# Kernel tuning notes

Hardware: AMD Instinct MI355X
Metric: run time of the kernel (lower is better)

## Reference

```python
import jax, jax.numpy as jnp
import numpy as np

N_BLADES = 8
GRADE = np.array([0, 1, 1, 1, 2, 2, 2, 3])
WEIGHT_EXPANSION = np.array([0, 1, 1, 1, 2, 2, 2, 3])
GRADE_BLADES = ([0], [1, 2, 3], [4, 5, 6], [7])
EPS = 1e-6


def _build_cayley():
    # Blades as bitmasks over generators e1,e2,e3; canonical order = sorted by (grade, mask)
    # -> [1, e1, e2, e3, e12, e13, e23, e123], matching weight_expansion [0,1,1,1,2,2,2,3].
    masks = sorted(range(8), key=lambda m: (bin(m).count('1'), m))
    m2i = {m: i for i, m in enumerate(masks)}
    ti, tj, tk, ts, triples = [], [], [], [], []
    for i, a in enumerate(masks):
        for j, b in enumerate(masks):
            # reorder sign for Euclidean Cl(3,0): count transpositions
            swaps = sum(bin(a >> (bit + 1)).count('1') for bit in range(3) if (b >> bit) & 1)
            k = m2i[a ^ b]
            ti.append(i); tj.append(j); tk.append(k)
            ts.append(-1.0 if swaps % 2 else 1.0)
            triples.append((int(GRADE[i]), int(GRADE[j]), int(GRADE[k])))
    uniq = sorted(set(triples))  # 20 directed grade-interaction paths for P3M0
    pidx = {t: p for p, t in enumerate(uniq)}
    tp = np.array([pidx[t] for t in triples])
    return (np.array(ti), np.array(tj), np.array(tk),
            np.array(ts, dtype=np.float32), tp, len(uniq))


TI, TJ, TK, TS, TP, NUM_PATHS = _build_cayley()  # NUM_PATHS == 20


def _forward(x, linear_weight, linear_bias, gp_weight, normalize=True):
    # grade-wise linear map via blade-expanded weights: y[k] = x[k] @ W[grade(k)] + b
    y = jnp.einsum('kbi,kio->kbo', x, linear_weight[WEIGHT_EXPANSION]) + linear_bias
    y = jax.nn.gelu(y, approximate=True)
    # steerable weighted geometric product: one learnable weight per feature per grade path
    wpath = gp_weight.T[TP]  # [64, F]: path weight for each blade-product term
    terms = (TS[:, None, None] * wpath[:, None, :]) * x[TI] * y[TJ]  # [64, B, F]
    out = jax.ops.segment_sum(terms, TK, num_segments=N_BLADES)  # [8, B, F]
    if normalize:
        # grade-wise RMS norm: per sample, normalize each grade subspace over its blades and features
        parts = []
        for blades in GRADE_BLADES:
            og = out[np.array(blades)]  # [n_blades_g, B, F]
            rms = jnp.sqrt(jnp.mean(og * og, axis=(0, 2), keepdims=True) + EPS)
            parts.append(og / rms)
        out = jnp.concatenate(parts, axis=0)
    return out


def setup_inputs() -> dict:
    key = jax.random.key(0)
    k1, k2, k3 = jax.random.split(key, 3)
    B, F = 4096, 512
    x = jax.random.normal(k1, (N_BLADES, B, F), dtype=jnp.float32)
    gp_weight = jax.random.normal(k2, (F, NUM_PATHS), dtype=jnp.float32) * np.float32(1.0 / np.sqrt(3 + 1))
    linear_weight = jax.random.normal(k3, (4, F, F), dtype=jnp.float32) * np.float32(1.0 / np.sqrt(F))
    linear_bias = jnp.zeros((1, 1, F), dtype=jnp.float32)
    return {"x": x, "linear_weight": linear_weight, "linear_bias": linear_bias, "gp_weight": gp_weight}


def reference(x, linear_weight, linear_bias, gp_weight):
    return _forward(x, linear_weight, linear_bias, gp_weight, normalize=True)
```

## Files before the change

### kernel.cpp

```cpp
#include <hip/hip_runtime.h>

typedef short short8v __attribute__((ext_vector_type(8)));
typedef float f32x4 __attribute__((ext_vector_type(4)));
typedef unsigned short u16;
typedef unsigned int u32;

__device__ __forceinline__ u16 f2bf(float f) {
    u32 u = __float_as_uint(f);
    u += 0x7FFFu + ((u >> 16) & 1u);
    return (u16)(u >> 16);
}
__device__ __forceinline__ float bf2f(u16 h) {
    return __uint_as_float(((u32)h) << 16);
}
__device__ __forceinline__ float gelu_f(float v) {
    float u = 0.7978845608028654f * fmaf(0.044715f * v, v * v, v);
    return 0.5f * v * (1.0f + tanhf(u));
}
__device__ __forceinline__ void gload16(const void* g, void* l) {
    __builtin_amdgcn_global_load_lds(
        (const __attribute__((address_space(1))) u32*)g,
        (__attribute__((address_space(3))) u32*)l, 16, 0, 0);
}

__global__ __launch_bounds__(256) void k_prep(const float* __restrict__ x, u16* __restrict__ xb,
                                              const float* __restrict__ w, u16* __restrict__ wt) {
    const int bid = blockIdx.x, tid = threadIdx.x;
    if (bid < 8192) {
        int idx = bid * 256 + tid;
        const float4* in = (const float4*)x;
        float4 a = in[idx * 2], c = in[idx * 2 + 1];
        short8v s;
        s[0] = (short)f2bf(a.x); s[1] = (short)f2bf(a.y); s[2] = (short)f2bf(a.z); s[3] = (short)f2bf(a.w);
        s[4] = (short)f2bf(c.x); s[5] = (short)f2bf(c.y); s[6] = (short)f2bf(c.z); s[7] = (short)f2bf(c.w);
        *(short8v*)(xb + (size_t)idx * 8) = s;
    } else {
        __shared__ float t[32][33];
        int tb = bid - 8192;
        int g = tb >> 8, rem = tb & 255;
        int o0 = (rem & 15) * 32, i0 = (rem >> 4) * 32;
        int tx = tid & 31, ty4 = tid >> 5;
#pragma unroll
        for (int r = 0; r < 4; r++) {
            int ty = ty4 * 4 + r;
            t[ty][tx] = w[(size_t)g * 262144 + (size_t)(i0 + ty) * 512 + (o0 + tx)];
        }
        __syncthreads();
#pragma unroll
        for (int r = 0; r < 4; r++) {
            int ty = ty4 * 4 + r;
            wt[(size_t)g * 262144 + (size_t)(o0 + ty) * 512 + (i0 + tx)] = f2bf(t[tx][ty]);
        }
    }
}

__global__ __launch_bounds__(256) void k_gemm(const u16* __restrict__ xb, const u16* __restrict__ wt,
                                              const float* __restrict__ bias, u16* __restrict__ yb) {
    __shared__ __align__(16) u16 sA[2][128 * 64];
    __shared__ __align__(16) u16 sB[2][128 * 64];
    const int tid = threadIdx.x;
    const int w = tid >> 6, lane = tid & 63;
    const int bid = blockIdx.x;
    const int swz = (bid & 7) * 128 + (bid >> 3);
    const int mt = swz >> 2, nt = swz & 3;
    const int WE[8] = {0, 1, 1, 1, 2, 2, 2, 3};
    const int g = WE[mt >> 5];
    const u16* Abase = xb + (size_t)mt * 128 * 512;
    const u16* Bbase = wt + (size_t)g * 262144 + (size_t)nt * 128 * 512;
    const int wr = w >> 1, wc = w & 1;
    const int lr = lane >> 3;
    const int lc = (lane & 7) * 16;

    f32x4 acc[4][4];
#pragma unroll
    for (int m = 0; m < 4; m++)
#pragma unroll
        for (int n = 0; n < 4; n++) acc[m][n] = (f32x4){0.f, 0.f, 0.f, 0.f};

#define STAGE(BUF, KT) { \
    _Pragma("unroll") \
    for (int p = 0; p < 4; ++p) { \
        int chunk = w * 4 + p; \
        gload16((const char*)(Abase + ((size_t)(chunk * 8 + lr) * 512 + (KT) * 64)) + lc, \
                (char*)sA[BUF] + chunk * 1024); \
        gload16((const char*)(Bbase + ((size_t)(chunk * 8 + lr) * 512 + (KT) * 64)) + lc, \
                (char*)sB[BUF] + chunk * 1024); \
    } }

#define COMPUTE(BUF) { \
    _Pragma("unroll") \
    for (int kk = 0; kk < 2; ++kk) { \
        short8v af[4], bfr[4]; \
        const int ko = kk * 64 + ((lane >> 4) * 16); \
        _Pragma("unroll") \
        for (int m = 0; m < 4; m++) { \
            int row = wr * 64 + m * 16 + (lane & 15); \
            af[m] = *(const short8v*)((const char*)sA[BUF] + row * 128 + ko); \
        } \
        _Pragma("unroll") \
        for (int n = 0; n < 4; n++) { \
            int col = wc * 64 + n * 16 + (lane & 15); \
            bfr[n] = *(const short8v*)((const char*)sB[BUF] + col * 128 + ko); \
        } \
        _Pragma("unroll") \
        for (int m = 0; m < 4; m++) \
            _Pragma("unroll") \
            for (int n = 0; n < 4; n++) \
                acc[m][n] = __builtin_amdgcn_mfma_f32_16x16x32_bf16(af[m], bfr[n], acc[m][n], 0, 0, 0); \
    } }

    STAGE(0, 0);
    __syncthreads();
    for (int kt = 0; kt < 6; kt += 2) {
        STAGE(1, kt + 1);
        COMPUTE(0);
        __syncthreads();
        STAGE(0, kt + 2);
        COMPUTE(1);
        __syncthreads();
    }
    STAGE(1, 7);
    COMPUTE(0);
    __syncthreads();
    COMPUTE(1);
#undef STAGE
#undef COMPUTE

    const size_t row0 = (size_t)mt * 128 + wr * 64;
    const int colBase = nt * 128 + wc * 64;
#pragma unroll
    for (int n = 0; n < 4; n++) {
        int col = colBase + n * 16 + (lane & 15);
        float bv = bias[col];
#pragma unroll
        for (int m = 0; m < 4; m++) {
#pragma unroll
            for (int j = 0; j < 4; j++) {
                size_t row = row0 + m * 16 + (lane >> 4) * 4 + j;
                float v = acc[m][n][j] + bv;
                yb[row * 512 + col] = f2bf(gelu_f(v));
            }
        }
    }
}

#define TERM(i, j, k, s, p) o[ff][k] = fmaf(s * wp[ff][p], xv[ff][i] * yv[ff][j], o[ff][k]);
#define GP_ALL \
    TERM(0,0,0, 1.0f,0) TERM(0,1,1, 1.0f,1) TERM(0,2,2, 1.0f,1) TERM(0,3,3, 1.0f,1) \
    TERM(0,4,4, 1.0f,2) TERM(0,5,5, 1.0f,2) TERM(0,6,6, 1.0f,2) TERM(0,7,7, 1.0f,3) \
    TERM(1,0,1, 1.0f,4) TERM(1,1,0, 1.0f,5) TERM(1,2,4, 1.0f,6) TERM(1,3,5, 1.0f,6) \
    TERM(1,4,2, 1.0f,7) TERM(1,5,3, 1.0f,7) TERM(1,6,7, 1.0f,8) TERM(1,7,6, 1.0f,9) \
    TERM(2,0,2, 1.0f,4) TERM(2,1,4,-1.0f,6) TERM(2,2,0, 1.0f,5) TERM(2,3,6, 1.0f,6) \
    TERM(2,4,1,-1.0f,7) TERM(2,5,7,-1.0f,8) TERM(2,6,3, 1.0f,7) TERM(2,7,5,-1.0f,9) \
    TERM(3,0,3, 1.0f,4) TERM(3,1,5,-1.0f,6) TERM(3,2,6,-1.0f,6) TERM(3,3,0, 1.0f,5) \
    TERM(3,4,7, 1.0f,8) TERM(3,5,1,-1.0f,7) TERM(3,6,2,-1.0f,7) TERM(3,7,4, 1.0f,9) \
    TERM(4,0,4, 1.0f,10) TERM(4,1,2,-1.0f,11) TERM(4,2,1, 1.0f,11) TERM(4,3,7, 1.0f,12) \
    TERM(4,4,0,-1.0f,13) TERM(4,5,6,-1.0f,14) TERM(4,6,5, 1.0f,14) TERM(4,7,3,-1.0f,15) \
    TERM(5,0,5, 1.0f,10) TERM(5,1,3,-1.0f,11) TERM(5,2,7,-1.0f,12) TERM(5,3,1, 1.0f,11) \
    TERM(5,4,6, 1.0f,14) TERM(5,5,0,-1.0f,13) TERM(5,6,4,-1.0f,14) TERM(5,7,2, 1.0f,15) \
    TERM(6,0,6, 1.0f,10) TERM(6,1,7, 1.0f,12) TERM(6,2,3,-1.0f,11) TERM(6,3,2, 1.0f,11) \
    TERM(6,4,5,-1.0f,14) TERM(6,5,4, 1.0f,14) TERM(6,6,0,-1.0f,13) TERM(6,7,1,-1.0f,15) \
    TERM(7,0,7, 1.0f,16) TERM(7,1,6, 1.0f,17) TERM(7,2,5,-1.0f,17) TERM(7,3,4, 1.0f,17) \
    TERM(7,4,3,-1.0f,18) TERM(7,5,2, 1.0f,18) TERM(7,6,1,-1.0f,18) TERM(7,7,0,-1.0f,19)

__global__ __launch_bounds__(256) void k_gp(const u16* __restrict__ xb, const u16* __restrict__ yb,
                                            const float* __restrict__ gp, float* __restrict__ out) {
    const int b = blockIdx.x, tid = threadIdx.x;
    const int w = tid >> 6, lane = tid & 63;
    const int f0 = tid * 2;

    float xv[2][8], yv[2][8], wp[2][20], o[2][8];
#pragma unroll
    for (int i = 0; i < 8; i++) {
        u32 ux = *(const u32*)(xb + ((size_t)i * 4096 + b) * 512 + f0);
        xv[0][i] = bf2f((u16)(ux & 0xFFFF)); xv[1][i] = bf2f((u16)(ux >> 16));
        u32 uy = *(const u32*)(yb + ((size_t)i * 4096 + b) * 512 + f0);
        yv[0][i] = bf2f((u16)(uy & 0xFFFF)); yv[1][i] = bf2f((u16)(uy >> 16));
    }
#pragma unroll
    for (int ff = 0; ff < 2; ++ff) {
        const float4* gv = (const float4*)(gp + (size_t)(f0 + ff) * 20);
#pragma unroll
        for (int q = 0; q < 5; ++q) {
            float4 v = gv[q];
            wp[ff][q * 4 + 0] = v.x; wp[ff][q * 4 + 1] = v.y;
            wp[ff][q * 4 + 2] = v.z; wp[ff][q * 4 + 3] = v.w;
        }
    }

    float ss[4] = {0.f, 0.f, 0.f, 0.f};
#pragma unroll
    for (int ff = 0; ff < 2; ++ff) {
#pragma unroll
        for (int k = 0; k < 8; k++) o[ff][k] = 0.f;
        GP_ALL
        ss[0] += o[ff][0] * o[ff][0];
        ss[1] += o[ff][1] * o[ff][1] + o[ff][2] * o[ff][2] + o[ff][3] * o[ff][3];
        ss[2] += o[ff][4] * o[ff][4] + o[ff][5] * o[ff][5] + o[ff][6] * o[ff][6];
        ss[3] += o[ff][7] * o[ff][7];
    }

#pragma unroll
    for (int g2 = 0; g2 < 4; g2++) {
        float v = ss[g2];
#pragma unroll
        for (int off = 32; off >= 1; off >>= 1) v += __shfl_xor(v, off);
        ss[g2] = v;
    }
    __shared__ float red[4][4];
    if (lane == 0) { red[w][0] = ss[0]; red[w][1] = ss[1]; red[w][2] = ss[2]; red[w][3] = ss[3]; }
    __syncthreads();
    float inv[4];
    const float cnt[4] = {512.f, 1536.f, 1536.f, 512.f};
#pragma unroll
    for (int g2 = 0; g2 < 4; g2++) {
        float tot = red[0][g2] + red[1][g2] + red[2][g2] + red[3][g2];
        inv[g2] = 1.0f / sqrtf(tot / cnt[g2] + 1e-6f);
    }
    const int GK[8] = {0, 1, 1, 1, 2, 2, 2, 3};
#pragma unroll
    for (int k = 0; k < 8; k++) {
        float2 st;
        st.x = o[0][k] * inv[GK[k]];
        st.y = o[1][k] * inv[GK[k]];
        *(float2*)(out + ((size_t)k * 4096 + b) * 512 + f0) = st;
    }
}

extern "C" void kernel_launch(void* const* d_in, const int* in_sizes, int n_in,
                              void* d_out, int out_size, void* d_ws, size_t ws_size,
                              hipStream_t stream) {
    const float* x  = (const float*)d_in[0];
    const float* lw = (const float*)d_in[1];
    const float* lb = (const float*)d_in[2];
    const float* gp = (const float*)d_in[3];
    float* out = (float*)d_out;
    char* ws = (char*)d_ws;
    u16* xb = (u16*)ws;
    u16* wt = (u16*)(ws + 33554432);
    u16* yb = (u16*)(ws + 35651584);

    hipLaunchKernelGGL(k_prep, dim3(9216), dim3(256), 0, stream, x, xb, lw, wt);
    hipLaunchKernelGGL(k_gemm, dim3(1024), dim3(256), 0, stream, xb, wt, lb, yb);
    hipLaunchKernelGGL(k_gp, dim3(4096), dim3(256), 0, stream, xb, yb, gp, out);
}
```

Baseline: 197.7 us.

## Enlarge GEMM tiles to 256x256 with 512 threads and K-step 32

Rewrites the bf16 MFMA GEMM so each block computes a 256x256 output tile with 8 waves (each doing 128x64), and stages 32-wide K slices instead of 64. The grid shrinks from 1024 blocks to 256 and the block-index swizzle is dropped. Larger tiles raise arithmetic intensity and reuse of each loaded A/B tile. In exchange, 256 blocks on a 256-CU part may leave occupancy thin, the K loop has twice as many barriers, and the 32-element LDS row stride may cause bank conflicts.

```diff
diff --git a/kernel.cpp b/kernel.cpp
--- a/kernel.cpp
+++ b/kernel.cpp
@@ -54,64 +54,57 @@
     }
 }
 
-__global__ __launch_bounds__(256) void k_gemm(const u16* __restrict__ xb, const u16* __restrict__ wt,
-                                              const float* __restrict__ bias, u16* __restrict__ yb) {
-    __shared__ __align__(16) u16 sA[2][128 * 64];
-    __shared__ __align__(16) u16 sB[2][128 * 64];
+__global__ __launch_bounds__(512, 2) void k_gemm(const u16* __restrict__ xb, const u16* __restrict__ wt,
+                                                 const float* __restrict__ bias, u16* __restrict__ yb) {
+    __shared__ __align__(16) u16 sA[2][256 * 32];
+    __shared__ __align__(16) u16 sB[2][256 * 32];
     const int tid = threadIdx.x;
     const int w = tid >> 6, lane = tid & 63;
-    const int bid = blockIdx.x;
-    const int swz = (bid & 7) * 128 + (bid >> 3);
-    const int mt = swz >> 2, nt = swz & 3;
+    const int mt = blockIdx.x, nt = blockIdx.y;
     const int WE[8] = {0, 1, 1, 1, 2, 2, 2, 3};
-    const int g = WE[mt >> 5];
-    const u16* Abase = xb + (size_t)mt * 128 * 512;
-    const u16* Bbase = wt + (size_t)g * 262144 + (size_t)nt * 128 * 512;
-    const int wr = w >> 1, wc = w & 1;
-    const int lr = lane >> 3;
-    const int lc = (lane & 7) * 16;
-
-    f32x4 acc[4][4];
-#pragma unroll
-    for (int m = 0; m < 4; m++)
+    const int g = WE[mt >> 4];
+    const char* Abase = (const char*)xb + (size_t)mt * 262144;
+    const char* Bbase = (const char*)wt + (size_t)g * 524288 + (size_t)nt * 262144;
+    const int wr = w >> 2, wc = w & 3;
+
+    f32x4 acc[8][4];
+#pragma unroll
+    for (int m = 0; m < 8; m++)
 #pragma unroll
         for (int n = 0; n < 4; n++) acc[m][n] = (f32x4){0.f, 0.f, 0.f, 0.f};
 
 #define STAGE(BUF, KT) { \
     _Pragma("unroll") \
-    for (int p = 0; p < 4; ++p) { \
-        int chunk = w * 4 + p; \
-        gload16((const char*)(Abase + ((size_t)(chunk * 8 + lr) * 512 + (KT) * 64)) + lc, \
-                (char*)sA[BUF] + chunk * 1024); \
-        gload16((const char*)(Bbase + ((size_t)(chunk * 8 + lr) * 512 + (KT) * 64)) + lc, \
-                (char*)sB[BUF] + chunk * 1024); \
+    for (int q = 0; q < 2; ++q) { \
+        int cid = q * 512 + tid; \
+        size_t goff = (size_t)(cid >> 2) * 1024 + (KT) * 64 + (cid & 3) * 16; \
+        gload16(Abase + goff, (char*)sA[BUF] + cid * 16); \
+        gload16(Bbase + goff, (char*)sB[BUF] + cid * 16); \
     } }
 
 #define COMPUTE(BUF) { \
-    _Pragma("unroll") \
-    for (int kk = 0; kk < 2; ++kk) { \
-        short8v af[4], bfr[4]; \
-        const int ko = kk * 64 + ((lane >> 4) * 16); \
+    short8v af[8], bfr[4]; \
+    const int ko = (lane >> 4) * 16; \
+    _Pragma("unroll") \
+    for (int m = 0; m < 8; m++) { \
+        int row = wr * 128 + m * 16 + (lane & 15); \
+        af[m] = *(const short8v*)((const char*)sA[BUF] + row * 64 + ko); \
+    } \
+    _Pragma("unroll") \
+    for (int n = 0; n < 4; n++) { \
+        int col = wc * 64 + n * 16 + (lane & 15); \
+        bfr[n] = *(const short8v*)((const char*)sB[BUF] + col * 64 + ko); \
+    } \
+    _Pragma("unroll") \
+    for (int m = 0; m < 8; m++) \
         _Pragma("unroll") \
-        for (int m = 0; m < 4; m++) { \
-            int row = wr * 64 + m * 16 + (lane & 15); \
-            af[m] = *(const short8v*)((const char*)sA[BUF] + row * 128 + ko); \
-        } \
-        _Pragma("unroll") \
-        for (int n = 0; n < 4; n++) { \
-            int col = wc * 64 + n * 16 + (lane & 15); \
-            bfr[n] = *(const short8v*)((const char*)sB[BUF] + col * 128 + ko); \
-        } \
-        _Pragma("unroll") \
-        for (int m = 0; m < 4; m++) \
-            _Pragma("unroll") \
-            for (int n = 0; n < 4; n++) \
-                acc[m][n] = __builtin_amdgcn_mfma_f32_16x16x32_bf16(af[m], bfr[n], acc[m][n], 0, 0, 0); \
-    } }
+        for (int n = 0; n < 4; n++) \
+            acc[m][n] = __builtin_amdgcn_mfma_f32_16x16x32_bf16(af[m], bfr[n], acc[m][n], 0, 0, 0); \
+    }
 
     STAGE(0, 0);
     __syncthreads();
-    for (int kt = 0; kt < 6; kt += 2) {
+    for (int kt = 0; kt < 14; kt += 2) {
         STAGE(1, kt + 1);
         COMPUTE(0);
         __syncthreads();
@@ -119,21 +112,21 @@
         COMPUTE(1);
         __syncthreads();
     }
-    STAGE(1, 7);
+    STAGE(1, 15);
     COMPUTE(0);
     __syncthreads();
     COMPUTE(1);
 #undef STAGE
 #undef COMPUTE
 
-    const size_t row0 = (size_t)mt * 128 + wr * 64;
-    const int colBase = nt * 128 + wc * 64;
+    const size_t row0 = (size_t)mt * 256 + wr * 128;
+    const int colBase = nt * 256 + wc * 64;
 #pragma unroll
     for (int n = 0; n < 4; n++) {
         int col = colBase + n * 16 + (lane & 15);
         float bv = bias[col];
 #pragma unroll
-        for (int m = 0; m < 4; m++) {
+        for (int m = 0; m < 8; m++) {
 #pragma unroll
             for (int j = 0; j < 4; j++) {
                 size_t row = row0 + m * 16 + (lane >> 4) * 4 + j;
@@ -241,6 +234,6 @@
     u16* yb = (u16*)(ws + 35651584);
 
     hipLaunchKernelGGL(k_prep, dim3(9216), dim3(256), 0, stream, x, xb, lw, wt);
-    hipLaunchKernelGGL(k_gemm, dim3(1024), dim3(256), 0, stream, xb, wt, lb, yb);
+    hipLaunchKernelGGL(k_gemm, dim3(128, 2), dim3(512), 0, stream, xb, wt, lb, yb);
     hipLaunchKernelGGL(k_gp, dim3(4096), dim3(256), 0, stream, xb, yb, gp, out);
 }
```

Result: faster. 193.8 us (-2.0%).

## Pre-pack operands into MFMA fragment layout and load GEMM fragments directly

Applied to the files above, without the earlier changes.

The prep kernel now writes x and the weights in a layout already matching the 16x16x32 MFMA fragment order, so each lane reads one contiguous 16-byte chunk per fragment. The GEMM drops its LDS staging and barriers and instead double-buffers fragments in registers loaded straight from global memory. The weight prep loses its shared-memory transpose in favour of strided scalar reads, and the GP kernel reads fp32 x directly instead of the bf16 copy. Without LDS, the A and B tiles shared across waves are fetched separately by each wave, which raises L2 traffic. Removing the block swizzle may also hurt cache locality.

```diff
diff --git a/kernel.cpp b/kernel.cpp
--- a/kernel.cpp
+++ b/kernel.cpp
@@ -17,59 +17,47 @@
     float u = 0.7978845608028654f * fmaf(0.044715f * v, v * v, v);
     return 0.5f * v * (1.0f + tanhf(u));
 }
-__device__ __forceinline__ void gload16(const void* g, void* l) {
-    __builtin_amdgcn_global_load_lds(
-        (const __attribute__((address_space(1))) u32*)g,
-        (__attribute__((address_space(3))) u32*)l, 16, 0, 0);
-}
-
-__global__ __launch_bounds__(256) void k_prep(const float* __restrict__ x, u16* __restrict__ xb,
-                                              const float* __restrict__ w, u16* __restrict__ wt) {
+
+__global__ __launch_bounds__(256) void k_prep(const float* __restrict__ x, u16* __restrict__ xpk,
+                                              const float* __restrict__ w, u16* __restrict__ wpk) {
     const int bid = blockIdx.x, tid = threadIdx.x;
     if (bid < 8192) {
-        int idx = bid * 256 + tid;
-        const float4* in = (const float4*)x;
-        float4 a = in[idx * 2], c = in[idx * 2 + 1];
+        int t = bid * 256 + tid;
+        int lane = t & 63, kb = (t >> 6) & 15, r16 = t >> 10;
+        int row = r16 * 16 + (lane & 15);
+        int k0 = kb * 32 + (lane >> 4) * 8;
+        const float4* src = (const float4*)(x + (size_t)row * 512 + k0);
+        float4 a = src[0], c = src[1];
         short8v s;
         s[0] = (short)f2bf(a.x); s[1] = (short)f2bf(a.y); s[2] = (short)f2bf(a.z); s[3] = (short)f2bf(a.w);
         s[4] = (short)f2bf(c.x); s[5] = (short)f2bf(c.y); s[6] = (short)f2bf(c.z); s[7] = (short)f2bf(c.w);
-        *(short8v*)(xb + (size_t)idx * 8) = s;
+        *(short8v*)(xpk + (size_t)t * 8) = s;
     } else {
-        __shared__ float t[32][33];
-        int tb = bid - 8192;
-        int g = tb >> 8, rem = tb & 255;
-        int o0 = (rem & 15) * 32, i0 = (rem >> 4) * 32;
-        int tx = tid & 31, ty4 = tid >> 5;
-#pragma unroll
-        for (int r = 0; r < 4; r++) {
-            int ty = ty4 * 4 + r;
-            t[ty][tx] = w[(size_t)g * 262144 + (size_t)(i0 + ty) * 512 + (o0 + tx)];
-        }
-        __syncthreads();
-#pragma unroll
-        for (int r = 0; r < 4; r++) {
-            int ty = ty4 * 4 + r;
-            wt[(size_t)g * 262144 + (size_t)(o0 + ty) * 512 + (i0 + tx)] = f2bf(t[tx][ty]);
-        }
-    }
-}
-
-__global__ __launch_bounds__(256) void k_gemm(const u16* __restrict__ xb, const u16* __restrict__ wt,
+        int t = (bid - 8192) * 256 + tid;
+        int lane = t & 63, kb = (t >> 6) & 15, c16 = (t >> 10) & 31, g = t >> 15;
+        int col = c16 * 16 + (lane & 15);
+        int k0 = kb * 32 + (lane >> 4) * 8;
+        const float* src = w + (size_t)g * 262144 + (size_t)k0 * 512 + col;
+        short8v s;
+#pragma unroll
+        for (int j = 0; j < 8; j++) s[j] = (short)f2bf(src[(size_t)j * 512]);
+        *(short8v*)(wpk + (size_t)t * 8) = s;
+    }
+}
+
+__global__ __launch_bounds__(256) void k_gemm(const u16* __restrict__ xpk, const u16* __restrict__ wpk,
                                               const float* __restrict__ bias, u16* __restrict__ yb) {
-    __shared__ __align__(16) u16 sA[2][128 * 64];
-    __shared__ __align__(16) u16 sB[2][128 * 64];
     const int tid = threadIdx.x;
     const int w = tid >> 6, lane = tid & 63;
     const int bid = blockIdx.x;
-    const int swz = (bid & 7) * 128 + (bid >> 3);
-    const int mt = swz >> 2, nt = swz & 3;
+    const int mt = bid >> 2, nt = bid & 3;
     const int WE[8] = {0, 1, 1, 1, 2, 2, 2, 3};
     const int g = WE[mt >> 5];
-    const u16* Abase = xb + (size_t)mt * 128 * 512;
-    const u16* Bbase = wt + (size_t)g * 262144 + (size_t)nt * 128 * 512;
     const int wr = w >> 1, wc = w & 1;
-    const int lr = lane >> 3;
-    const int lc = (lane & 7) * 16;
+    const int loff = lane * 16;
+
+    const char* Ab = (const char*)xpk + (size_t)(mt * 8 + wr * 4) * 16384 + loff;
+    const char* Bb = (const char*)wpk + (size_t)(g * 32 + nt * 8 + wc * 4) * 16384 + loff;
 
     f32x4 acc[4][4];
 #pragma unroll
@@ -77,54 +65,35 @@
 #pragma unroll
         for (int n = 0; n < 4; n++) acc[m][n] = (f32x4){0.f, 0.f, 0.f, 0.f};
 
-#define STAGE(BUF, KT) { \
+    short8v a0[4], b0[4], a1[4], b1[4];
+
+#define LOADF(AR, BR, KB) { \
     _Pragma("unroll") \
-    for (int p = 0; p < 4; ++p) { \
-        int chunk = w * 4 + p; \
-        gload16((const char*)(Abase + ((size_t)(chunk * 8 + lr) * 512 + (KT) * 64)) + lc, \
-                (char*)sA[BUF] + chunk * 1024); \
-        gload16((const char*)(Bbase + ((size_t)(chunk * 8 + lr) * 512 + (KT) * 64)) + lc, \
-                (char*)sB[BUF] + chunk * 1024); \
-    } }
-
-#define COMPUTE(BUF) { \
+    for (int m = 0; m < 4; m++) AR[m] = *(const short8v*)(Ab + (size_t)m * 16384 + (KB) * 1024); \
     _Pragma("unroll") \
-    for (int kk = 0; kk < 2; ++kk) { \
-        short8v af[4], bfr[4]; \
-        const int ko = kk * 64 + ((lane >> 4) * 16); \
+    for (int n = 0; n < 4; n++) BR[n] = *(const short8v*)(Bb + (size_t)n * 16384 + (KB) * 1024); \
+    }
+#define MM(AR, BR) { \
+    _Pragma("unroll") \
+    for (int m = 0; m < 4; m++) \
         _Pragma("unroll") \
-        for (int m = 0; m < 4; m++) { \
-            int row = wr * 64 + m * 16 + (lane & 15); \
-            af[m] = *(const short8v*)((const char*)sA[BUF] + row * 128 + ko); \
-        } \
-        _Pragma("unroll") \
-        for (int n = 0; n < 4; n++) { \
-            int col = wc * 64 + n * 16 + (lane & 15); \
-            bfr[n] = *(const short8v*)((const char*)sB[BUF] + col * 128 + ko); \
-        } \
-        _Pragma("unroll") \
-        for (int m = 0; m < 4; m++) \
-            _Pragma("unroll") \
-            for (int n = 0; n < 4; n++) \
-                acc[m][n] = __builtin_amdgcn_mfma_f32_16x16x32_bf16(af[m], bfr[n], acc[m][n], 0, 0, 0); \
-    } }
-
-    STAGE(0, 0);
-    __syncthreads();
-    for (int kt = 0; kt < 6; kt += 2) {
-        STAGE(1, kt + 1);
-        COMPUTE(0);
-        __syncthreads();
-        STAGE(0, kt + 2);
-        COMPUTE(1);
-        __syncthreads();
-    }
-    STAGE(1, 7);
-    COMPUTE(0);
-    __syncthreads();
-    COMPUTE(1);
-#undef STAGE
-#undef COMPUTE
+        for (int n = 0; n < 4; n++) \
+            acc[m][n] = __builtin_amdgcn_mfma_f32_16x16x32_bf16(AR[m], BR[n], acc[m][n], 0, 0, 0); \
+    }
+
+    LOADF(a0, b0, 0);
+#pragma unroll
+    for (int kb = 0; kb < 14; kb += 2) {
+        LOADF(a1, b1, kb + 1);
+        MM(a0, b0);
+        LOADF(a0, b0, kb + 2);
+        MM(a1, b1);
+    }
+    LOADF(a1, b1, 15);
+    MM(a0, b0);
+    MM(a1, b1);
+#undef LOADF
+#undef MM
 
     const size_t row0 = (size_t)mt * 128 + wr * 64;
     const int colBase = nt * 128 + wc * 64;
@@ -163,7 +132,7 @@
     TERM(7,0,7, 1.0f,16) TERM(7,1,6, 1.0f,17) TERM(7,2,5,-1.0f,17) TERM(7,3,4, 1.0f,17) \
     TERM(7,4,3,-1.0f,18) TERM(7,5,2, 1.0f,18) TERM(7,6,1,-1.0f,18) TERM(7,7,0,-1.0f,19)
 
-__global__ __launch_bounds__(256) void k_gp(const u16* __restrict__ xb, const u16* __restrict__ yb,
+__global__ __launch_bounds__(256) void k_gp(const float* __restrict__ x, const u16* __restrict__ yb,
                                             const float* __restrict__ gp, float* __restrict__ out) {
     const int b = blockIdx.x, tid = threadIdx.x;
     const int w = tid >> 6, lane = tid & 63;
@@ -172,8 +141,8 @@
     float xv[2][8], yv[2][8], wp[2][20], o[2][8];
 #pragma unroll
     for (int i = 0; i < 8; i++) {
-        u32 ux = *(const u32*)(xb + ((size_t)i * 4096 + b) * 512 + f0);
-        xv[0][i] = bf2f((u16)(ux & 0xFFFF)); xv[1][i] = bf2f((u16)(ux >> 16));
+        float2 xf = *(const float2*)(x + ((size_t)i * 4096 + b) * 512 + f0);
+        xv[0][i] = xf.x; xv[1][i] = xf.y;
         u32 uy = *(const u32*)(yb + ((size_t)i * 4096 + b) * 512 + f0);
         yv[0][i] = bf2f((u16)(uy & 0xFFFF)); yv[1][i] = bf2f((u16)(uy >> 16));
     }
@@ -236,11 +205,11 @@
     const float* gp = (const float*)d_in[3];
     float* out = (float*)d_out;
     char* ws = (char*)d_ws;
-    u16* xb = (u16*)ws;
-    u16* wt = (u16*)(ws + 33554432);
-    u16* yb = (u16*)(ws + 35651584);
-
-    hipLaunchKernelGGL(k_prep, dim3(9216), dim3(256), 0, stream, x, xb, lw, wt);
-    hipLaunchKernelGGL(k_gemm, dim3(1024), dim3(256), 0, stream, xb, wt, lb, yb);
-    hipLaunchKernelGGL(k_gp, dim3(4096), dim3(256), 0, stream, xb, yb, gp, out);
-}
+    u16* xpk = (u16*)ws;
+    u16* wpk = (u16*)(ws + 33554432);
+    u16* yb  = (u16*)(ws + 35651584);
+
+    hipLaunchKernelGGL(k_prep, dim3(8704), dim3(256), 0, stream, x, xpk, lw, wpk);
+    hipLaunchKernelGGL(k_gemm, dim3(1024), dim3(256), 0, stream, xpk, wpk, lb, yb);
+    hipLaunchKernelGGL(k_gp, dim3(4096), dim3(256), 0, stream, x, yb, gp, out);
+}
```

Result: no change. 196.8 us (-0.4%).
